# Optimization experiments

Hardware: AMD Instinct MI355X
Metric: run time of the kernel (lower is better)

Reference implementation:

```python
import jax, jax.numpy as jnp
import numpy as np

D_MODEL = 1024
NUM_HEADS = 16
HEAD_DIMS = D_MODEL // NUM_HEADS


def setup_inputs() -> dict:
    key = jax.random.key(0)
    k1, k2, k3, k4, k5 = jax.random.split(key, 5)
    B, S = 2, 2048
    x = jax.random.normal(k1, (B, S, D_MODEL), dtype=jnp.float32)
    mask = jnp.zeros((B, S, S), dtype=jnp.float32)  # additive float mask
    # torch Linear weights; stored as (in, out) so y = x @ W + b
    s_in = 1.0 / np.sqrt(D_MODEL)
    Wqkv = jax.random.uniform(k2, (D_MODEL, 3 * D_MODEL), jnp.float32, -s_in, s_in)
    bqkv = jax.random.uniform(k3, (3 * D_MODEL,), jnp.float32, -s_in, s_in)
    Wo = jax.random.uniform(k4, (D_MODEL, D_MODEL), jnp.float32, -s_in, s_in)
    bo = jax.random.uniform(k5, (D_MODEL,), jnp.float32, -s_in, s_in)
    return {"x": x, "mask": mask, "Wqkv": Wqkv, "bqkv": bqkv, "Wo": Wo, "bo": bo}


def reference(x, mask, Wqkv, bqkv, Wo, bo):
    B, S, _ = x.shape
    qkv = x @ Wqkv + bqkv                                   # [B, S, 3*D]
    qkv = qkv.reshape(B, S, NUM_HEADS, 3 * HEAD_DIMS)
    qkv = jnp.transpose(qkv, (0, 2, 1, 3))                  # [B, H, S, 3*hd]
    q, k, v = jnp.split(qkv, 3, axis=-1)                    # each [B, H, S, hd]
    scale = 1.0 / np.sqrt(HEAD_DIMS).astype(np.float32)
    scores = jnp.einsum("bhqd,bhkd->bhqk", q, k) * scale    # [B, H, S, S]
    scores = scores + mask[:, None, :, :]
    attn = jax.nn.softmax(scores, axis=-1)
    values = jnp.einsum("bhqk,bhkd->bhqd", attn, v)         # [B, H, S, hd]
    # Faithful to original: direct row-major reshape (B,H,S,hd)->(B,S,H*hd),
    # WITHOUT transposing heads back (replicates the source's reshape).
    values = values.reshape(B, S, NUM_HEADS * HEAD_DIMS)
    out = values @ Wo + bo
    return out
```

## Files before the change

kernel.cpp:

```cpp
#include <hip/hip_runtime.h>
#include <stdint.h>


#define LOG2E 1.44269504088896340736f

typedef __attribute__((ext_vector_type(4))) float f32x4;
typedef __attribute__((ext_vector_type(8))) short short8v;
typedef __attribute__((ext_vector_type(4))) short short4v;
typedef __attribute__((ext_vector_type(8))) __bf16 bf16x8;
typedef __attribute__((ext_vector_type(2))) __bf16 bf16x2;
typedef __attribute__((ext_vector_type(4))) unsigned uint4v;

__device__ __forceinline__ unsigned short f2bf(float f) {
  unsigned u = __builtin_bit_cast(unsigned, f);
  u += 0x7FFFu + ((u >> 16) & 1u);
  return (unsigned short)(u >> 16);
}

__device__ __forceinline__ unsigned pack2(float lo, float hi) {
  return (unsigned)f2bf(lo) | ((unsigned)f2bf(hi) << 16);
}

__device__ __forceinline__ unsigned packbf(float lo, float hi) {
  bf16x2 t;
  t[0] = (__bf16)lo;
  t[1] = (__bf16)hi;
  return __builtin_bit_cast(unsigned, t);
}

__device__ __forceinline__ f32x4 mfma16(short8v a, short8v b, f32x4 c) {
  return __builtin_amdgcn_mfma_f32_16x16x32_bf16(
      __builtin_bit_cast(bf16x8, a), __builtin_bit_cast(bf16x8, b), c, 0, 0, 0);
}

__device__ __forceinline__ void gload_lds16(const void* g, void* l) {
  __builtin_amdgcn_global_load_lds(
      (const __attribute__((address_space(1))) void*)(uintptr_t)g,
      (__attribute__((address_space(3))) void*)(uintptr_t)l, 16, 0, 0);
}

__global__ void cvt_x_kernel(const float4* __restrict__ src,
                             uint2* __restrict__ dst, int n4) {
  int i = blockIdx.x * 256 + threadIdx.x;
  if (i < n4) {
    float4 v = src[i];
    dst[i] = make_uint2(pack2(v.x, v.y), pack2(v.z, v.w));
  }
}

__global__ void transpose_cvt_kernel(const float* __restrict__ src,
                                     unsigned short* __restrict__ dst,
                                     int R, int C) {
  __shared__ unsigned short tile[64][65];
  int tc = threadIdx.x & 63;
  int tr = threadIdx.x >> 6;
  int c0 = blockIdx.x * 64;
  int r0 = blockIdx.y * 64;
#pragma unroll
  for (int i = 0; i < 16; ++i) {
    int r = tr * 16 + i;
    tile[r][tc] = f2bf(src[(size_t)(r0 + r) * C + c0 + tc]);
  }
  __syncthreads();
#pragma unroll
  for (int i = 0; i < 16; ++i) {
    int cc = tr * 16 + i;
    dst[(size_t)(c0 + cc) * R + r0 + tc] = tile[tc][cc];
  }
}

__global__ __launch_bounds__(256, 2)
void gemm_qkv_kernel(const unsigned short* __restrict__ xbf,
                     const unsigned short* __restrict__ WT,
                     const float* __restrict__ bias,
                     unsigned short* __restrict__ Qb,
                     unsigned short* __restrict__ Kb,
                     unsigned short* __restrict__ VbT) {
  const int K = 1024;
  __shared__ __align__(16) unsigned short As[128 * 64];
  __shared__ __align__(16) unsigned short Bs[128 * 64];
  int tid = threadIdx.x;
  int lane = tid & 63;
  int wid = tid >> 6;
  int m0 = blockIdx.y * 128;
  int n0 = blockIdx.x * 128;
  int wm = (wid >> 1) * 64;
  int wn = (wid & 1) * 64;
  f32x4 acc[4][4] = {};
  for (int k0 = 0; k0 < K; k0 += 64) {
#pragma unroll
    for (int it = 0; it < 4; ++it) {
      int G = it * 256 + tid;
      int r = G >> 3, g = G & 7;
      int sg = g ^ (r & 7);
      gload_lds16(xbf + (size_t)(m0 + r) * K + k0 + sg * 8, &As[G * 8]);
      gload_lds16(WT + (size_t)(n0 + r) * K + k0 + sg * 8, &Bs[G * 8]);
    }
    __syncthreads();
#pragma unroll
    for (int ks = 0; ks < 2; ++ks) {
      short8v a[4], bf[4];
      int kg = ks * 4 + (lane >> 4);
#pragma unroll
      for (int i = 0; i < 4; ++i) {
        int ra = wm + i * 16 + (lane & 15);
        a[i] = *(const short8v*)&As[ra * 64 + ((kg ^ (ra & 7)) << 3)];
        int rb = wn + i * 16 + (lane & 15);
        bf[i] = *(const short8v*)&Bs[rb * 64 + ((kg ^ (rb & 7)) << 3)];
      }
#pragma unroll
      for (int i = 0; i < 4; ++i)
#pragma unroll
        for (int j = 0; j < 4; ++j)
          acc[i][j] = mfma16(a[i], bf[j], acc[i][j]);
    }
    __syncthreads();
  }
#pragma unroll
  for (int i = 0; i < 4; ++i) {
#pragma unroll
    for (int j = 0; j < 4; ++j) {
      int n = n0 + wn + j * 16 + (lane & 15);
      float bv = bias[n];
      int h = n / 192;
      int rr = n - h * 192;
      int t = rr >> 6;
      int d = rr & 63;
#pragma unroll
      for (int rg = 0; rg < 4; ++rg) {
        int m = m0 + wm + i * 16 + ((lane >> 4) << 2) + rg;
        int b = m >> 11, s = m & 2047;
        unsigned short val = f2bf(acc[i][j][rg] + bv);
        int bh = b * 16 + h;
        if (t == 2) {
          VbT[((size_t)bh * 64 + d) * 2048 + s] = val;
        } else {
          unsigned short* dst = (t == 0) ? Qb : Kb;
          dst[((size_t)bh * 2048 + s) * 64 + d] = val;
        }
      }
    }
  }
}


#define ATTN_STAGE(kt_, bi_)                                                  \
  do {                                                                        \
    _Pragma("unroll") for (int it_ = 0; it_ < 2; ++it_) {                     \
      int G_ = it_ * 256 + tid;                                               \
      int r_ = G_ >> 3, g_ = G_ & 7;                                          \
      int sg_ = g_ ^ (r_ & 7);                                                \
      gload_lds16(Kb + bh_off + (size_t)((kt_)*64 + r_) * 64 + sg_ * 8,       \
                  &Ks[bi_][G_ * 8]);                                          \
      gload_lds16(VbT + bh_off + (size_t)r_ * 2048 + (kt_)*64 + sg_ * 8,      \
                  &Vs[bi_][G_ * 8]);                                          \
    }                                                                         \
  } while (0)

#define ATTN_TILE(kt_, CUR_)                                                  \
  do {                                                                        \
    if ((kt_) < 31) ATTN_STAGE((kt_) + 1, (CUR_) ^ 1);                        \
                \
    f32x4 mk_[4];                                                             \
    _Pragma("unroll") for (int f = 0; f < 4; ++f)                             \
        mk_[f] = *(const f32x4*)(mrowq + (size_t)(kt_)*64 + f * 16);          \
                            \
    f32x4 sf[4] = {};                                                         \
    _Pragma("unroll") for (int ks = 0; ks < 2; ++ks) {                        \
      short8v qa = ks ? qa1 : qa0;                                            \
      int kg = ks * 4 + hi;                                                   \
      _Pragma("unroll") for (int f = 0; f < 4; ++f) {                         \
        int row = f * 16 + lq;                                                \
        short8v kb =                                                          \
            *(const short8v*)&Ks[CUR_][row * 64 + ((kg ^ (row & 7)) << 3)];   \
        sf[f] = mfma16(kb, qa, sf[f]);                                        \
      }                                                                       \
    }                                                                         \
    _Pragma("unroll") for (int f = 0; f < 4; ++f)                             \
        _Pragma("unroll") for (int r = 0; r < 4; ++r)                         \
            sf[f][r] = fmaf(sf[f][r], 0.125f, mk_[f][r]);                     \
                 \
    float mx0_ = fmaxf(fmaxf(sf[0][0], sf[0][1]), fmaxf(sf[0][2], sf[0][3])); \
    float mx1_ = fmaxf(fmaxf(sf[1][0], sf[1][1]), fmaxf(sf[1][2], sf[1][3])); \
    float mx2_ = fmaxf(fmaxf(sf[2][0], sf[2][1]), fmaxf(sf[2][2], sf[2][3])); \
    float mx3_ = fmaxf(fmaxf(sf[3][0], sf[3][1]), fmaxf(sf[3][2], sf[3][3])); \
    float mt_ = fmaxf(fmaxf(mx0_, mx1_), fmaxf(mx2_, mx3_));                  \
    mt_ = fmaxf(mt_, __shfl_xor(mt_, 16));                                    \
    mt_ = fmaxf(mt_, __shfl_xor(mt_, 32));                                    \
                                                               \
    if (!__all(mt_ <= m_s + THR)) {                                           \
      float mn_ = fmaxf(m_s, mt_);                                            \
      float al_ = exp2f((m_s - mn_) * LOG2E);                                 \
      m_s = mn_;                                                              \
      mLs = mn_ * LOG2E;                                                      \
      l_s *= al_;                                                             \
      float a0_ = __shfl(al_, (lane & 48) | hi4);                             \
      float a1_ = __shfl(al_, (lane & 48) | (hi4 + 1));                       \
      float a2_ = __shfl(al_, (lane & 48) | (hi4 + 2));                       \
      float a3_ = __shfl(al_, (lane & 48) | (hi4 + 3));                       \
      _Pragma("unroll") for (int f = 0; f < 4; ++f) {                         \
        o[f][0] *= a0_; o[f][1] *= a1_; o[f][2] *= a2_; o[f][3] *= a3_;       \
      }                                                                       \
    }                                                                         \
            \
    unsigned pk_[4][2];                                                       \
    _Pragma("unroll") for (int f = 0; f < 4; ++f) {                           \
      float p0_ = exp2f(fmaf(sf[f][0], LOG2E, -mLs));                         \
      float p1_ = exp2f(fmaf(sf[f][1], LOG2E, -mLs));                         \
      float p2_ = exp2f(fmaf(sf[f][2], LOG2E, -mLs));                         \
      float p3_ = exp2f(fmaf(sf[f][3], LOG2E, -mLs));                         \
      l_s += (p0_ + p1_) + (p2_ + p3_);                                       \
      pk_[f][0] = packbf(p0_, p1_);                                           \
      pk_[f][1] = packbf(p2_, p3_);                                           \
    }                                                                         \
    \
    \
    _Pragma("unroll") for (int ks = 0; ks < 2; ++ks) {                        \
      uint4v au_;                                                             \
      au_[0] = pk_[2 * ks][0];                                                \
      au_[1] = pk_[2 * ks][1];                                                \
      au_[2] = pk_[2 * ks + 1][0];                                            \
      au_[3] = pk_[2 * ks + 1][1];                                            \
      short8v pa = __builtin_bit_cast(short8v, au_);                          \
      _Pragma("unroll") for (int f = 0; f < 4; ++f) {                         \
        int vrow_ = f * 16 + lq;                                              \
        int blkA_ = 4 * ks + (hi >> 1);                                       \
        int eA_ = vrow_ * 64 + (((blkA_) ^ (vrow_ & 7)) << 3) +               \
                  ((hi & 1) << 2);                                            \
        int eB_ = vrow_ * 64 + (((blkA_ + 2) ^ (vrow_ & 7)) << 3) +           \
                  ((hi & 1) << 2);                                            \
        short4v vlo_ = *(const short4v*)&Vs[CUR_][eA_];                       \
        short4v vhi_ = *(const short4v*)&Vs[CUR_][eB_];                       \
        short8v vb_;                                                          \
        vb_[0] = vlo_[0]; vb_[1] = vlo_[1]; vb_[2] = vlo_[2];                 \
        vb_[3] = vlo_[3]; vb_[4] = vhi_[0]; vb_[5] = vhi_[1];                 \
        vb_[6] = vhi_[2]; vb_[7] = vhi_[3];                                   \
        o[f] = mfma16(pa, vb_, o[f]);                                         \
      }                                                                       \
    }                                                                         \
    __syncthreads();                                                          \
  } while (0)

__global__ __launch_bounds__(256, 4)
void attn_kernel(const unsigned short* __restrict__ Qb,
                 const unsigned short* __restrict__ Kb,
                 const unsigned short* __restrict__ VbT,
                 const float* __restrict__ mask,
                 unsigned short* __restrict__ vals) {
  __shared__ __align__(16) unsigned short Ks[2][64 * 64];
  __shared__ __align__(16) unsigned short Vs[2][64 * 64];
  int tid = threadIdx.x;
  int lane = tid & 63;
  int wid = tid >> 6;
  int lq = lane & 15;
  int hi = lane >> 4;
  int hi4 = hi << 2;
  int h = blockIdx.x & 15;
  int qt = (blockIdx.x >> 4) & 31;
  int b = blockIdx.x >> 9;
  int bh = b * 16 + h;
  size_t bh_off = (size_t)bh * 2048 * 64;
  int q0 = qt * 64 + wid * 16;

  const unsigned short* qptr =
      Qb + bh_off + (size_t)(q0 + lq) * 64 + (hi << 3);
  short8v qa0 = *(const short8v*)qptr;
  short8v qa1 = *(const short8v*)(qptr + 32);

  f32x4 o[4] = {};
  float m_s = -1e30f, l_s = 0.f, mLs = 0.f;

  const float* mrowq = mask + ((size_t)b * 2048 + q0 + lq) * 2048 + hi4;

  const float THR = 4.0f;

  ATTN_STAGE(0, 0);
  __syncthreads();

  for (int t = 0; t < 16; ++t) {
    ATTN_TILE(2 * t, 0);
    ATTN_TILE(2 * t + 1, 1);
  }

  l_s += __shfl_xor(l_s, 16);
  l_s += __shfl_xor(l_s, 32);
  float ri_ = 1.0f / l_s;
  float rv_[4];
#pragma unroll
  for (int r = 0; r < 4; ++r) rv_[r] = __shfl(ri_, (lane & 48) | (hi4 + r));

#pragma unroll
  for (int f = 0; f < 4; ++f)
#pragma unroll
    for (int r = 0; r < 4; ++r) {
      int s = q0 + hi4 + r;
      int d = f * 16 + lq;
      int s2 = h * 128 + (s >> 4);
      int c2 = ((s & 15) << 6) + d;
      vals[((size_t)b * 2048 + s2) * 1024 + c2] = f2bf(o[f][r] * rv_[r]);
    }
}

__global__ __launch_bounds__(256, 2)
void gemm_out_kernel(const unsigned short* __restrict__ vals,
                     const unsigned short* __restrict__ WoT,
                     const float* __restrict__ bo,
                     float* __restrict__ out) {
  const int K = 1024;
  __shared__ __align__(16) unsigned short As[128 * 64];
  __shared__ __align__(16) unsigned short Bs[128 * 64];
  int tid = threadIdx.x;
  int lane = tid & 63;
  int wid = tid >> 6;
  int m0 = blockIdx.y * 128;
  int n0 = blockIdx.x * 128;
  int wm = (wid >> 1) * 64;
  int wn = (wid & 1) * 64;
  f32x4 acc[4][4] = {};
  for (int k0 = 0; k0 < K; k0 += 64) {
#pragma unroll
    for (int it = 0; it < 4; ++it) {
      int G = it * 256 + tid;
      int r = G >> 3, g = G & 7;
      int sg = g ^ (r & 7);
      gload_lds16(vals + (size_t)(m0 + r) * K + k0 + sg * 8, &As[G * 8]);
      gload_lds16(WoT + (size_t)(n0 + r) * K + k0 + sg * 8, &Bs[G * 8]);
    }
    __syncthreads();
#pragma unroll
    for (int ks = 0; ks < 2; ++ks) {
      short8v a[4], bf[4];
      int kg = ks * 4 + (lane >> 4);
#pragma unroll
      for (int i = 0; i < 4; ++i) {
        int ra = wm + i * 16 + (lane & 15);
        a[i] = *(const short8v*)&As[ra * 64 + ((kg ^ (ra & 7)) << 3)];
        int rb = wn + i * 16 + (lane & 15);
        bf[i] = *(const short8v*)&Bs[rb * 64 + ((kg ^ (rb & 7)) << 3)];
      }
#pragma unroll
      for (int i = 0; i < 4; ++i)
#pragma unroll
        for (int j = 0; j < 4; ++j)
          acc[i][j] = mfma16(a[i], bf[j], acc[i][j]);
    }
    __syncthreads();
  }
#pragma unroll
  for (int i = 0; i < 4; ++i) {
#pragma unroll
    for (int j = 0; j < 4; ++j) {
      int n = n0 + wn + j * 16 + (lane & 15);
      float bv = bo[n];
#pragma unroll
      for (int rg = 0; rg < 4; ++rg) {
        int m = m0 + wm + i * 16 + ((lane >> 4) << 2) + rg;
        out[(size_t)m * 1024 + n] = acc[i][j][rg] + bv;
      }
    }
  }
}

extern "C" void kernel_launch(void* const* d_in, const int* in_sizes, int n_in,
                              void* d_out, int out_size, void* d_ws,
                              size_t ws_size, hipStream_t stream) {
  const float* x    = (const float*)d_in[0];
  const float* mask = (const float*)d_in[1];
  const float* Wqkv = (const float*)d_in[2];
  const float* bqkv = (const float*)d_in[3];
  const float* Wo   = (const float*)d_in[4];
  const float* bo   = (const float*)d_in[5];
  float* out = (float*)d_out;

  char* ws = (char*)d_ws;
  unsigned short* xbf   = (unsigned short*)(ws);
  unsigned short* WqkvT = (unsigned short*)(ws + 8388608);
  unsigned short* WoT   = (unsigned short*)(ws + 14680064);
  unsigned short* Qb    = (unsigned short*)(ws + 16777216);
  unsigned short* Kb    = (unsigned short*)(ws + 25165824);
  unsigned short* VbT   = (unsigned short*)(ws + 33554432);
  unsigned short* vals  = xbf;

  hipLaunchKernelGGL(cvt_x_kernel, dim3(4096), dim3(256), 0, stream,
                     (const float4*)x, (uint2*)xbf, 1048576);
  hipLaunchKernelGGL(transpose_cvt_kernel, dim3(48, 16), dim3(256), 0, stream,
                     Wqkv, WqkvT, 1024, 3072);
  hipLaunchKernelGGL(transpose_cvt_kernel, dim3(16, 16), dim3(256), 0, stream,
                     Wo, WoT, 1024, 1024);
  hipLaunchKernelGGL(gemm_qkv_kernel, dim3(24, 32), dim3(256), 0, stream,
                     xbf, WqkvT, bqkv, Qb, Kb, VbT);
  hipLaunchKernelGGL(attn_kernel, dim3(1024), dim3(256), 0, stream,
                     Qb, Kb, VbT, mask, vals);
  hipLaunchKernelGGL(gemm_out_kernel, dim3(8, 32), dim3(256), 0, stream,
                     vals, WoT, bo, out);
}
```

Baseline: 252.7 us.

## Double-buffer output GEMM with narrower tiles; shuffle P so V loads are 16-byte

In the output projection GEMM, the kernel now uses double-buffered LDS with prefetch of the next K-slice, and halves the N tile to 64 so twice as many blocks launch. In attention, the bf16 probability fragments are rearranged across lanes with shuffles so that each V operand becomes one 16-byte LDS read instead of two 8-byte reads plus repacking. The aim is to hide global-load latency in the GEMM, improve occupancy across the GPU, and cut LDS instructions in the PV MMA. The cost is eight extra shuffles per k-step in attention and less data reuse per GEMM block.

```diff
diff --git a/kernel.cpp b/kernel.cpp
--- a/kernel.cpp
+++ b/kernel.cpp
@@ -6,7 +6,6 @@
 
 typedef __attribute__((ext_vector_type(4))) float f32x4;
 typedef __attribute__((ext_vector_type(8))) short short8v;
-typedef __attribute__((ext_vector_type(4))) short short4v;
 typedef __attribute__((ext_vector_type(8))) __bf16 bf16x8;
 typedef __attribute__((ext_vector_type(2))) __bf16 bf16x2;
 typedef __attribute__((ext_vector_type(4))) unsigned uint4v;
@@ -213,28 +212,30 @@
       pk_[f][0] = packbf(p0_, p1_);                                           \
       pk_[f][1] = packbf(p2_, p3_);                                           \
     }                                                                         \
-    \
-    \
+     \
+     \
+     \
+     \
     _Pragma("unroll") for (int ks = 0; ks < 2; ++ks) {                        \
+      unsigned s0_ = __shfl(pk_[2 * ks][0], sha_);                            \
+      unsigned s1_ = __shfl(pk_[2 * ks][1], sha_);                            \
+      unsigned s2_ = __shfl(pk_[2 * ks][0], shb_);                            \
+      unsigned s3_ = __shfl(pk_[2 * ks][1], shb_);                            \
+      unsigned t0_ = __shfl(pk_[2 * ks + 1][0], sha_);                        \
+      unsigned t1_ = __shfl(pk_[2 * ks + 1][1], sha_);                        \
+      unsigned t2_ = __shfl(pk_[2 * ks + 1][0], shb_);                        \
+      unsigned t3_ = __shfl(pk_[2 * ks + 1][1], shb_);                        \
       uint4v au_;                                                             \
-      au_[0] = pk_[2 * ks][0];                                                \
-      au_[1] = pk_[2 * ks][1];                                                \
-      au_[2] = pk_[2 * ks + 1][0];                                            \
-      au_[3] = pk_[2 * ks + 1][1];                                            \
+      au_[0] = hilo_ ? s0_ : t0_;                                             \
+      au_[1] = hilo_ ? s1_ : t1_;                                             \
+      au_[2] = hilo_ ? s2_ : t2_;                                             \
+      au_[3] = hilo_ ? s3_ : t3_;                                             \
       short8v pa = __builtin_bit_cast(short8v, au_);                          \
+      int kg = ks * 4 + hi;                                                   \
       _Pragma("unroll") for (int f = 0; f < 4; ++f) {                         \
         int vrow_ = f * 16 + lq;                                              \
-        int blkA_ = 4 * ks + (hi >> 1);                                       \
-        int eA_ = vrow_ * 64 + (((blkA_) ^ (vrow_ & 7)) << 3) +               \
-                  ((hi & 1) << 2);                                            \
-        int eB_ = vrow_ * 64 + (((blkA_ + 2) ^ (vrow_ & 7)) << 3) +           \
-                  ((hi & 1) << 2);                                            \
-        short4v vlo_ = *(const short4v*)&Vs[CUR_][eA_];                       \
-        short4v vhi_ = *(const short4v*)&Vs[CUR_][eB_];                       \
-        short8v vb_;                                                          \
-        vb_[0] = vlo_[0]; vb_[1] = vlo_[1]; vb_[2] = vlo_[2];                 \
-        vb_[3] = vlo_[3]; vb_[4] = vhi_[0]; vb_[5] = vhi_[1];                 \
-        vb_[6] = vhi_[2]; vb_[7] = vhi_[3];                                   \
+        short8v vb_ =                                                         \
+            *(const short8v*)&Vs[CUR_][vrow_ * 64 + ((kg ^ (vrow_ & 7)) << 3)]; \
         o[f] = mfma16(pa, vb_, o[f]);                                         \
       }                                                                       \
     }                                                                         \
@@ -255,6 +256,9 @@
   int lq = lane & 15;
   int hi = lane >> 4;
   int hi4 = hi << 2;
+  int sha_ = lq | ((hi & 1) << 5);
+  int shb_ = sha_ | 16;
+  bool hilo_ = (hi < 2);
   int h = blockIdx.x & 15;
   int qt = (blockIdx.x >> 4) & 31;
   int b = blockIdx.x >> 9;
@@ -301,60 +305,81 @@
     }
 }
 
+
+#define OUT_STAGE(k0_, bi_)                                                   \
+  do {                                                                        \
+    _Pragma("unroll") for (int it_ = 0; it_ < 4; ++it_) {                     \
+      int G_ = it_ * 256 + tid;                                               \
+      int r_ = G_ >> 3, g_ = G_ & 7;                                          \
+      int sg_ = g_ ^ (r_ & 7);                                                \
+      gload_lds16(vals + (size_t)(m0 + r_) * 1024 + (k0_) + sg_ * 8,          \
+                  &As[bi_][G_ * 8]);                                          \
+    }                                                                         \
+    _Pragma("unroll") for (int it_ = 0; it_ < 2; ++it_) {                     \
+      int G_ = it_ * 256 + tid;                                               \
+      int r_ = G_ >> 3, g_ = G_ & 7;                                          \
+      int sg_ = g_ ^ (r_ & 7);                                                \
+      gload_lds16(WoT + (size_t)(n0 + r_) * 1024 + (k0_) + sg_ * 8,           \
+                  &Bs[bi_][G_ * 8]);                                          \
+    }                                                                         \
+  } while (0)
+
+#define OUT_STEP(k0_, CUR_)                                                   \
+  do {                                                                        \
+    if ((k0_) + 64 < 1024) OUT_STAGE((k0_) + 64, (CUR_) ^ 1);                 \
+    _Pragma("unroll") for (int ks = 0; ks < 2; ++ks) {                        \
+      short8v a_[4], b_[2];                                                   \
+      int kg = ks * 4 + hi;                                                   \
+      _Pragma("unroll") for (int i = 0; i < 4; ++i) {                         \
+        int ra = wm + i * 16 + lq;                                            \
+        a_[i] = *(const short8v*)&As[CUR_][ra * 64 + ((kg ^ (ra & 7)) << 3)]; \
+      }                                                                       \
+      _Pragma("unroll") for (int j = 0; j < 2; ++j) {                         \
+        int rb = wn + j * 16 + lq;                                            \
+        b_[j] = *(const short8v*)&Bs[CUR_][rb * 64 + ((kg ^ (rb & 7)) << 3)]; \
+      }                                                                       \
+      _Pragma("unroll") for (int i = 0; i < 4; ++i)                           \
+          _Pragma("unroll") for (int j = 0; j < 2; ++j)                       \
+              acc[i][j] = mfma16(a_[i], b_[j], acc[i][j]);                    \
+    }                                                                         \
+    __syncthreads();                                                          \
+  } while (0)
+
 __global__ __launch_bounds__(256, 2)
 void gemm_out_kernel(const unsigned short* __restrict__ vals,
                      const unsigned short* __restrict__ WoT,
                      const float* __restrict__ bo,
                      float* __restrict__ out) {
-  const int K = 1024;
-  __shared__ __align__(16) unsigned short As[128 * 64];
-  __shared__ __align__(16) unsigned short Bs[128 * 64];
+  __shared__ __align__(16) unsigned short As[2][128 * 64];
+  __shared__ __align__(16) unsigned short Bs[2][64 * 64];
   int tid = threadIdx.x;
   int lane = tid & 63;
   int wid = tid >> 6;
+  int lq = lane & 15;
+  int hi = lane >> 4;
   int m0 = blockIdx.y * 128;
-  int n0 = blockIdx.x * 128;
+  int n0 = blockIdx.x * 64;
   int wm = (wid >> 1) * 64;
-  int wn = (wid & 1) * 64;
-  f32x4 acc[4][4] = {};
-  for (int k0 = 0; k0 < K; k0 += 64) {
-#pragma unroll
-    for (int it = 0; it < 4; ++it) {
-      int G = it * 256 + tid;
-      int r = G >> 3, g = G & 7;
-      int sg = g ^ (r & 7);
-      gload_lds16(vals + (size_t)(m0 + r) * K + k0 + sg * 8, &As[G * 8]);
-      gload_lds16(WoT + (size_t)(n0 + r) * K + k0 + sg * 8, &Bs[G * 8]);
-    }
-    __syncthreads();
-#pragma unroll
-    for (int ks = 0; ks < 2; ++ks) {
-      short8v a[4], bf[4];
-      int kg = ks * 4 + (lane >> 4);
-#pragma unroll
-      for (int i = 0; i < 4; ++i) {
-        int ra = wm + i * 16 + (lane & 15);
-        a[i] = *(const short8v*)&As[ra * 64 + ((kg ^ (ra & 7)) << 3)];
-        int rb = wn + i * 16 + (lane & 15);
-        bf[i] = *(const short8v*)&Bs[rb * 64 + ((kg ^ (rb & 7)) << 3)];
-      }
-#pragma unroll
-      for (int i = 0; i < 4; ++i)
-#pragma unroll
-        for (int j = 0; j < 4; ++j)
-          acc[i][j] = mfma16(a[i], bf[j], acc[i][j]);
-    }
-    __syncthreads();
-  }
+  int wn = (wid & 1) * 32;
+  f32x4 acc[4][2] = {};
+
+  OUT_STAGE(0, 0);
+  __syncthreads();
+#pragma unroll 1
+  for (int kk = 0; kk < 8; ++kk) {
+    OUT_STEP(kk * 128, 0);
+    OUT_STEP(kk * 128 + 64, 1);
+  }
+
 #pragma unroll
   for (int i = 0; i < 4; ++i) {
 #pragma unroll
-    for (int j = 0; j < 4; ++j) {
-      int n = n0 + wn + j * 16 + (lane & 15);
+    for (int j = 0; j < 2; ++j) {
+      int n = n0 + wn + j * 16 + lq;
       float bv = bo[n];
 #pragma unroll
       for (int rg = 0; rg < 4; ++rg) {
-        int m = m0 + wm + i * 16 + ((lane >> 4) << 2) + rg;
+        int m = m0 + wm + i * 16 + (hi << 2) + rg;
         out[(size_t)m * 1024 + n] = acc[i][j][rg] + bv;
       }
     }
@@ -391,6 +416,6 @@
                      xbf, WqkvT, bqkv, Qb, Kb, VbT);
   hipLaunchKernelGGL(attn_kernel, dim3(1024), dim3(256), 0, stream,
                      Qb, Kb, VbT, mask, vals);
-  hipLaunchKernelGGL(gemm_out_kernel, dim3(8, 32), dim3(256), 0, stream,
+  hipLaunchKernelGGL(gemm_out_kernel, dim3(16, 32), dim3(256), 0, stream,
                      vals, WoT, bo, out);
 }
```

Result: slower. 258.1 us (+2.1%).
